# Kernel optimization log

Hardware: AMD Instinct MI355X
Metric: run time of the kernel (lower is better)

Reference implementation:

```python
import jax, jax.numpy as jnp
import numpy as np

B, C, M = 2048, 1, 80  # M = max_object; matrices are (M+1)x(M+1)


def setup_inputs() -> dict:
    key = jax.random.key(0)
    k1, k2, k3, k4 = jax.random.split(key, 4)
    inp = {
        "input": jax.random.normal(k1, (B, C, M + 1, M + 1), dtype=jnp.float32),
        "target": jax.random.randint(k2, (B, C, M + 1, M + 1), 0, 2, dtype=jnp.int32),
        "mask0": jax.random.randint(k3, (B, C, M + 1), 0, 2, dtype=jnp.int32),
        "mask1": jax.random.randint(k4, (B, C, M + 1), 0, 2, dtype=jnp.int32),
        "outputs": 0,
        "current_fair_labels": 0,
        "next_fair_labels": 0,
    }
    return inp


def reference(input, target, mask0, mask1, outputs, current_fair_labels, next_fair_labels):
    f32 = jnp.float32
    m0 = mask0.astype(f32)[:, :, :, None]   # [B,C,M+1,1] (row mask, broadcast over cols)
    m1 = mask1.astype(f32)[:, :, None, :]   # [B,C,1,M+1] (col mask, broadcast over rows)
    mask_region = m0 * m1                    # [B,C,M+1,M+1]
    mask_region_pre = mask_region.at[:, :, M, :].set(0.0)   # zero last row
    mask_region_next = mask_region.at[:, :, :, M].set(0.0)  # zero last col
    mask_region_union = mask_region_pre * mask_region_next

    input_pre = jax.nn.softmax(mask_region_pre * input, axis=3)
    input_next = jax.nn.softmax(mask_region_next * input, axis=2)
    input_all = input_pre.at[:, :, :M, :M].set(
        jnp.maximum(input_pre, input_next)[:, :, :M, :M])

    t = target.astype(jnp.bool_).astype(f32)
    target_pre = mask_region_pre * t
    target_next = mask_region_next * t
    target_union = mask_region_union * t

    target_num = t.sum()
    n_pre = target_pre.sum()
    n_next = target_next.sum()
    n_union = target_union.sum()

    s_pre = -(target_pre * jnp.log(input_pre)).sum()
    loss_pre = jnp.where(n_pre > 0, s_pre / n_pre, s_pre)

    s_next = -(target_next * jnp.log(input_next)).sum()
    loss_next = jnp.where(n_next > 0, s_next / n_next, s_next)

    s_all = -(target_pre * jnp.log(input_all)).sum()
    loss = jnp.where((n_pre > 0) & (n_next > 0), s_all / n_pre, s_all)

    # |1 - p_pre - (1 - p_next)| == |p_next - p_pre|
    s_sim = (target_union * jnp.abs(input_next - input_pre)).sum()
    loss_similarity = jnp.where(n_union > 0, s_sim / target_num, s_sim)

    # accuracy on "pre" direction (argmax over cols, drop last row)
    idx_t_pre = jnp.argmax(target_pre, axis=3)[:, :, :-1]
    indexes_pre = jnp.argmax(input_all, axis=3)[:, :, :-1]
    mpre = mask0.astype(f32)[:, :, :-1]
    n_mpre = mpre.sum()
    s_acc_pre = ((indexes_pre == idx_t_pre).astype(f32) * mpre).sum()
    accuracy_pre = jnp.where(n_mpre > 0, s_acc_pre / n_mpre, s_acc_pre + 1.0)

    # accuracy on "next" direction (argmax over rows, drop last col)
    idx_t_next = jnp.argmax(target_next, axis=2)[:, :, :-1]
    indexes_next = jnp.argmax(input_next, axis=2)[:, :, :-1]
    mnext = mask1.astype(f32)[:, :, :-1]
    n_mnext = mnext.sum()
    s_acc_next = ((indexes_next == idx_t_next).astype(f32) * mnext).sum()
    accuracy_next = jnp.where(n_mnext > 0, s_acc_next / n_mnext, s_acc_next + 1.0)

    total = (loss_pre + loss_next + loss + loss_similarity) / 4.0
    return (loss_pre, loss_next, loss_similarity, total,
            accuracy_pre, accuracy_next, (accuracy_pre + accuracy_next) / 2.0,
            indexes_pre)
```

## Files before the change

kernel.cpp:

```cpp
#include <hip/hip_runtime.h>

#define M1 81
#define MSZ 80
#define NEL (M1 * M1)
#define NTW ((NEL + 31) / 32)
#define NACC 12
#define BIGKC 1.0e30f
#define LOG81 4.394449154672439f
#define INV81 0.012345679012345678f


__global__ __launch_bounds__(512, 8) void sst_main(
    const float* __restrict__ input,
    const int* __restrict__ target,
    const int* __restrict__ mask0,
    const int* __restrict__ mask1,
    float* __restrict__ out_idx,
    float* __restrict__ part,
    int slices)
{
    __shared__ float s_x[NEL];
    __shared__ unsigned s_tb[NTW];
    __shared__ float s_m0[M1], s_m1[M1];
    __shared__ float s_kc[M1];
    __shared__ float s_invc[M1];
    __shared__ float s_pA[486];
    __shared__ float s_pC[480];
    __shared__ float s_pV[486];
    __shared__ unsigned char s_pI[486];
    __shared__ unsigned char s_pT[486];
    __shared__ unsigned s_m1w[4];
    __shared__ float s_wv[8][NACC];

    const int tid   = threadIdx.x;
    const int lane  = tid & 63;
    const int w     = tid >> 6;
    const int slice = blockIdx.x;
    const size_t base = (size_t)slice * NEL;

    if (tid < M1) s_m0[tid] = (float)mask0[slice * M1 + tid];
    else if (tid >= 128 && tid < 128 + M1) s_m1[tid - 128] = (float)mask1[slice * M1 + (tid - 128)];

    float a[NACC];
#pragma unroll
    for (int k = 0; k < NACC; ++k) a[k] = 0.0f;

    for (int i = tid; i < NEL; i += 512) {
        s_x[i] = input[base + i];
        const int tv = target[base + i];
        a[0] += (tv != 0) ? 1.0f : 0.0f;
        unsigned long long m = __ballot(tv != 0);
        if (lane == 0) {
            const int w2 = (i >> 5) & ~1;
            s_tb[w2] = (unsigned)m;
            if (w2 + 1 < NTW) s_tb[w2 + 1] = (unsigned)(m >> 32);
        }
    }
    __syncthreads();

    if (w == 0) {
        const unsigned long long m = __ballot(s_m1[lane] != 0.0f);
        if (lane == 0) { s_m1w[0] = (unsigned)m; s_m1w[1] = (unsigned)(m >> 32); }
    } else if (w == 1) {
        float v = 0.0f;
        if (lane < 17) v = s_m1[64 + lane];
        const unsigned long long m = __ballot(v != 0.0f);
        if (lane == 0) { s_m1w[2] = (unsigned)m; s_m1w[3] = 0u; }
    }

    if (tid < 486) {
        const int c = tid / 6, j = tid - 6 * (tid / 6);
        const int r0 = j * 13 + ((j < 3) ? j : 3);
        const int len = (j < 3) ? 14 : 13;
        const float m1c = s_m1[c];
        const float mcol = (c == MSZ) ? 0.0f : m1c;
        float cs = 0.0f, bv = -1.0f;
        int bi = r0, ct = 127;
        for (int i = 0; i < len; ++i) {
            const int r = r0 + i;
            const int idx = r * M1 + c;
            const float m0r = s_m0[r];
            const float z = m1c * m0r * s_x[idx];
            const float e = __expf(z);
            s_x[idx] = z;
            cs += e;
            if (e > bv) { bv = e; bi = r; }
            const unsigned tb = (s_tb[idx >> 5] >> (idx & 31)) & 1u;
            if (ct == 127 && tb != 0u && (mcol * m0r) != 0.0f) ct = r;
        }
        s_pA[tid] = cs; s_pV[tid] = bv;
        s_pI[tid] = (unsigned char)bi; s_pT[tid] = (unsigned char)ct;
    }
    __syncthreads();

    if (tid < 480) {
        const int r = tid / 6, j = tid - 6 * (tid / 6);
        const int c0 = j * 13 + ((j < 3) ? j : 3);
        const int len = (j < 3) ? 14 : 13;
        const int rb = r * M1 + c0;
        float rs = 0.0f;
        for (int i = 0; i < len; ++i) rs += __expf(s_x[rb + i]);
        s_pC[tid] = rs;
    } else {
        const int u = tid - 480;
        for (int c = u; c < M1; c += 32) {
            if (c < MSZ) {
                const int b = 6 * c;
                float cs = 0.0f;
#pragma unroll
                for (int k = 0; k < 6; ++k) cs += s_pA[b + k];
                float bv = s_pV[b]; int bi = s_pI[b];
#pragma unroll
                for (int k = 1; k < 6; ++k) {
                    const float v = s_pV[b + k];
                    if (v > bv) { bv = v; bi = s_pI[b + k]; }
                }
                int ct = 127;
#pragma unroll
                for (int k = 0; k < 6; ++k) ct = min(ct, (int)s_pT[b + k]);
                if (ct == 127) ct = 0;
                s_kc[c] = __logf(cs);
                s_invc[c] = 1.0f / cs;
                const float m1c = s_m1[c];
                a[9]  += (bi == ct) ? m1c : 0.0f;
                a[11] += m1c;
            } else {
                s_kc[c] = BIGKC; s_invc[c] = INV81;
            }
        }
    }
    __syncthreads();

    if (tid < 480) {
        const int r = tid / 6, j = tid - 6 * (tid / 6);
        const int c0 = j * 13 + ((j < 3) ? j : 3);
        const int len = (j < 3) ? 14 : 13;
        const int rb = r * M1;
        const int pb = 6 * r;
        const float rs = s_pC[pb] + s_pC[pb + 1] + s_pC[pb + 2]
                       + s_pC[pb + 3] + s_pC[pb + 4] + s_pC[pb + 5];
        const float lr = __logf(rs), invr = 1.0f / rs;
        const float m0f = s_m0[r];

        const int bp = rb + c0;
        const unsigned long long tw64 =
            ((unsigned long long)s_tb[(bp >> 5) + 1] << 32) | s_tb[bp >> 5];
        const int mp0 = c0 >> 5;
        const unsigned long long mw64 =
            ((unsigned long long)s_m1w[mp0 + 1] << 32) | s_m1w[mp0];
        const unsigned lenmask = (1u << len) - 1u;
        unsigned wb = (unsigned)(tw64 >> (bp & 31)) & (unsigned)(mw64 >> (c0 & 31)) & lenmask;
        if (m0f == 0.0f) wb = 0u;

        const unsigned w3 = (j == 5) ? (wb & 0x0FFFu) : wb;
        a[1] += (float)__popc(wb);
        a[2] += (float)__popc(w3);
        a[3] += (float)__popc(w3);
        const int ti = wb ? (c0 + __ffs(wb) - 1) : 127;

        float bv = -3.402823466e38f; int bi = c0;
        for (int i = 0; i < len; ++i) {
            const int c = c0 + i;
            const float val = s_x[rb + c] - fminf(lr, s_kc[c]);
            if (val > bv) { bv = val; bi = c; }
        }
        unsigned wl = wb;
        while (wl) {
            const int b = __ffs(wl) - 1; wl &= wl - 1u;
            const int c = c0 + b;
            const float z = s_x[rb + c];
            const float kc = s_kc[c];
            a[4] += lr - z;
            a[6] += fminf(lr, kc) - z;
            const bool c80 = (c == MSZ);
            a[5] += c80 ? 0.0f : (kc - z);
            const float e = c80 ? 0.0f : __expf(z);
            a[7] = fmaf(e, fabsf(s_invc[c] - invr), a[7]);
        }
        s_pV[tid] = bv; s_pI[tid] = (unsigned char)bi; s_pT[tid] = (unsigned char)ti;
    } else if (tid < 486) {
        const int j = tid - 480;
        const int c0 = j * 13 + ((j < 3) ? j : 3);
        const int len = (j < 3) ? 14 : 13;
        const int rb = MSZ * M1;
        const float m80 = s_m0[MSZ];
        const int bp = rb + c0;
        const unsigned long long tw64 =
            ((unsigned long long)s_tb[(bp >> 5) + 1] << 32) | s_tb[bp >> 5];
        const int mp0 = c0 >> 5;
        const unsigned long long mw64 =
            ((unsigned long long)s_m1w[mp0 + 1] << 32) | s_m1w[mp0];
        const unsigned lenmask = (1u << len) - 1u;
        unsigned wb = (unsigned)(tw64 >> (bp & 31)) & (unsigned)(mw64 >> (c0 & 31)) & lenmask;
        if (m80 == 0.0f) wb = 0u;
        if (j == 5) wb &= 0x0FFFu;
        a[2] += (float)__popc(wb);
        while (wb) {
            const int b = __ffs(wb) - 1; wb &= wb - 1u;
            const int c = c0 + b;
            a[5] += s_kc[c] - s_x[rb + c];
        }
    }
    __syncthreads();

    if (tid < MSZ) {
        const int b = 6 * tid;
        float bv = s_pV[b]; int bi = s_pI[b];
#pragma unroll
        for (int k = 1; k < 6; ++k) {
            const float v = s_pV[b + k];
            if (v > bv) { bv = v; bi = s_pI[b + k]; }
        }
        int ti = 127;
#pragma unroll
        for (int k = 0; k < 6; ++k) ti = min(ti, (int)s_pT[b + k]);
        if (ti == 127) ti = 0;
        out_idx[(size_t)slice * MSZ + tid] = (float)bi;
        const float m0f = s_m0[tid];
        a[8]  += (bi == ti) ? m0f : 0.0f;
        a[10] += m0f;
    }

#pragma unroll
    for (int k = 0; k < NACC; ++k) {
        float v = a[k];
        for (int off = 32; off > 0; off >>= 1) v += __shfl_down(v, off);
        if (lane == 0) s_wv[w][k] = v;
    }
    __syncthreads();
    if (tid < NACC) {
        float s = 0.0f;
#pragma unroll
        for (int ww = 0; ww < 8; ++ww) s += s_wv[ww][tid];
        part[(size_t)tid * slices + slice] = s;
    }
}

__global__ __launch_bounds__(256) void sst_final(
    const float* __restrict__ part, int slices, float* __restrict__ out)
{
    __shared__ double s_part[4][NACC];
    const int tid = threadIdx.x;
    double l[NACC];
#pragma unroll
    for (int k = 0; k < NACC; ++k) l[k] = 0.0;
    for (int s = tid; s < slices; s += 256) {
#pragma unroll
        for (int k = 0; k < NACC; ++k) l[k] += (double)part[(size_t)k * slices + s];
    }
#pragma unroll
    for (int k = 0; k < NACC; ++k) {
        double v = l[k];
        for (int off = 32; off > 0; off >>= 1) v += __shfl_down(v, off);
        if ((tid & 63) == 0) s_part[tid >> 6][k] = v;
    }
    __syncthreads();
    if (tid == 0) {
        double g[NACC];
#pragma unroll
        for (int k = 0; k < NACC; ++k)
            g[k] = s_part[0][k] + s_part[1][k] + s_part[2][k] + s_part[3][k];
        const double tnum = g[0], npre = g[1], nnext = g[2], nunion = g[3];
        const double spre = g[4], snext = g[5], sall = g[6], ssim = g[7];
        const double accp = g[8], accn = g[9], nmp = g[10], nmn = g[11];
        const double loss_pre  = (npre > 0.0) ? spre / npre : spre;
        const double loss_next = (nnext > 0.0) ? snext / nnext : snext;
        const double loss      = (npre > 0.0 && nnext > 0.0) ? sall / npre : sall;
        const double loss_sim  = (nunion > 0.0) ? ssim / tnum : ssim;
        const double total = (loss_pre + loss_next + loss + loss_sim) * 0.25;
        const double ap = (nmp > 0.0) ? accp / nmp : accp + 1.0;
        const double an = (nmn > 0.0) ? accn / nmn : accn + 1.0;
        out[0] = (float)loss_pre;
        out[1] = (float)loss_next;
        out[2] = (float)loss_sim;
        out[3] = (float)total;
        out[4] = (float)ap;
        out[5] = (float)an;
        out[6] = (float)((ap + an) * 0.5);
    }
}

extern "C" void kernel_launch(void* const* d_in, const int* in_sizes, int n_in,
                              void* d_out, int out_size, void* d_ws, size_t ws_size,
                              hipStream_t stream) {
    const float* input  = (const float*)d_in[0];
    const int*   target = (const int*)d_in[1];
    const int*   mask0  = (const int*)d_in[2];
    const int*   mask1  = (const int*)d_in[3];
    float* out = (float*)d_out;
    float* part = (float*)d_ws;

    const int slices = in_sizes[0] / NEL;

    sst_main<<<slices, 512, 0, stream>>>(input, target, mask0, mask1, out + 7, part, slices);
    sst_final<<<1, 256, 0, stream>>>(part, slices, out);
}
```

Baseline: 167.4 us.

## Vectorize input loads, store exp in shared memory, defer target bitmask build

The input tile is now loaded with aligned float4 reads, using a per-slice shared-memory offset so the vector loads line up. Target values are prefetched into registers and turned into the ballot bitmask after the column pass, so those loads overlap with compute. Shared memory now holds exp(z) instead of z, which removes the repeated exp in the row-sum pass at the cost of a log in the sparse target loop. The first target row of each column for the column accuracy now comes from shared-memory atomicMin during the row pass rather than a per-element bit test in the column pass. The atomics and the extra register pressure from 13 prefetched ints could hurt occupancy.

```diff
diff --git a/kernel.cpp b/kernel.cpp
--- a/kernel.cpp
+++ b/kernel.cpp
@@ -6,8 +6,6 @@
 #define NTW ((NEL + 31) / 32)
 #define NACC 12
 #define BIGKC 1.0e30f
-#define LOG81 4.394449154672439f
-#define INV81 0.012345679012345678f
 
 
 __global__ __launch_bounds__(512, 8) void sst_main(
@@ -19,7 +17,7 @@
     float* __restrict__ part,
     int slices)
 {
-    __shared__ float s_x[NEL];
+    __shared__ __align__(16) float s_xraw[NEL + 4];
     __shared__ unsigned s_tb[NTW];
     __shared__ float s_m0[M1], s_m1[M1];
     __shared__ float s_kc[M1];
@@ -29,6 +27,8 @@
     __shared__ float s_pV[486];
     __shared__ unsigned char s_pI[486];
     __shared__ unsigned char s_pT[486];
+    __shared__ unsigned char s_ci[MSZ];
+    __shared__ int s_ct[MSZ];
     __shared__ unsigned s_m1w[4];
     __shared__ float s_wv[8][NACC];
 
@@ -38,23 +38,29 @@
     const int slice = blockIdx.x;
     const size_t base = (size_t)slice * NEL;
 
+    float* sx = s_xraw + (slice & 3);
+    const int h = (4 - (slice & 3)) & 3;
+
     if (tid < M1) s_m0[tid] = (float)mask0[slice * M1 + tid];
     else if (tid >= 128 && tid < 128 + M1) s_m1[tid - 128] = (float)mask1[slice * M1 + (tid - 128)];
+    if (tid >= 256 && tid < 256 + MSZ) s_ct[tid - 256] = 0x7fffffff;
 
     float a[NACC];
 #pragma unroll
     for (int k = 0; k < NACC; ++k) a[k] = 0.0f;
 
-    for (int i = tid; i < NEL; i += 512) {
-        s_x[i] = input[base + i];
-        const int tv = target[base + i];
-        a[0] += (tv != 0) ? 1.0f : 0.0f;
-        unsigned long long m = __ballot(tv != 0);
-        if (lane == 0) {
-            const int w2 = (i >> 5) & ~1;
-            s_tb[w2] = (unsigned)m;
-            if (w2 + 1 < NTW) s_tb[w2 + 1] = (unsigned)(m >> 32);
-        }
+    const int n4 = (NEL - h) >> 2;
+    const float4* in4 = (const float4*)(input + base + h);
+    for (int i = tid; i < n4; i += 512)
+        *(float4*)(sx + h + (i << 2)) = in4[i];
+    if (tid < h) sx[tid] = input[base + tid];
+    for (int i = h + (n4 << 2) + tid; i < NEL; i += 512) sx[i] = input[base + i];
+
+    int tpre[13];
+#pragma unroll
+    for (int k = 0; k < 13; ++k) {
+        const int i = tid + (k << 9);
+        tpre[k] = (i < NEL) ? target[base + i] : 0;
     }
     __syncthreads();
 
@@ -73,23 +79,32 @@
         const int r0 = j * 13 + ((j < 3) ? j : 3);
         const int len = (j < 3) ? 14 : 13;
         const float m1c = s_m1[c];
-        const float mcol = (c == MSZ) ? 0.0f : m1c;
         float cs = 0.0f, bv = -1.0f;
-        int bi = r0, ct = 127;
-        for (int i = 0; i < len; ++i) {
+        int bi = r0;
+        int idx = r0 * M1 + c;
+        for (int i = 0; i < len; ++i, idx += M1) {
             const int r = r0 + i;
-            const int idx = r * M1 + c;
-            const float m0r = s_m0[r];
-            const float z = m1c * m0r * s_x[idx];
+            const float z = m1c * s_m0[r] * sx[idx];
             const float e = __expf(z);
-            s_x[idx] = z;
+            sx[idx] = e;
             cs += e;
             if (e > bv) { bv = e; bi = r; }
-            const unsigned tb = (s_tb[idx >> 5] >> (idx & 31)) & 1u;
-            if (ct == 127 && tb != 0u && (mcol * m0r) != 0.0f) ct = r;
-        }
-        s_pA[tid] = cs; s_pV[tid] = bv;
-        s_pI[tid] = (unsigned char)bi; s_pT[tid] = (unsigned char)ct;
+        }
+        s_pA[tid] = cs; s_pV[tid] = bv; s_pI[tid] = (unsigned char)bi;
+    }
+
+#pragma unroll
+    for (int k = 0; k < 13; ++k) {
+        const int i = tid + (k << 9);
+        if (i < NEL) {
+            const unsigned long long m = __ballot(tpre[k] != 0);
+            if (lane == 0) {
+                a[0] += (float)__popcll(m);
+                const int w2 = (i >> 5) & ~1;
+                s_tb[w2] = (unsigned)m;
+                if (w2 + 1 < NTW) s_tb[w2 + 1] = (unsigned)(m >> 32);
+            }
+        }
     }
     __syncthreads();
 
@@ -99,7 +114,7 @@
         const int len = (j < 3) ? 14 : 13;
         const int rb = r * M1 + c0;
         float rs = 0.0f;
-        for (int i = 0; i < len; ++i) rs += __expf(s_x[rb + i]);
+        for (int i = 0; i < len; ++i) rs += sx[rb + i];
         s_pC[tid] = rs;
     } else {
         const int u = tid - 480;
@@ -115,17 +130,12 @@
                     const float v = s_pV[b + k];
                     if (v > bv) { bv = v; bi = s_pI[b + k]; }
                 }
-                int ct = 127;
-#pragma unroll
-                for (int k = 0; k < 6; ++k) ct = min(ct, (int)s_pT[b + k]);
-                if (ct == 127) ct = 0;
                 s_kc[c] = __logf(cs);
                 s_invc[c] = 1.0f / cs;
-                const float m1c = s_m1[c];
-                a[9]  += (bi == ct) ? m1c : 0.0f;
-                a[11] += m1c;
+                s_ci[c] = (unsigned char)bi;
             } else {
-                s_kc[c] = BIGKC; s_invc[c] = INV81;
+                s_kc[c] = BIGKC;
+                s_invc[c] = 0.0f;
             }
         }
     }
@@ -158,24 +168,25 @@
         a[3] += (float)__popc(w3);
         const int ti = wb ? (c0 + __ffs(wb) - 1) : 127;
 
-        float bv = -3.402823466e38f; int bi = c0;
+        float bv = -1.0f; int bi = c0;
         for (int i = 0; i < len; ++i) {
             const int c = c0 + i;
-            const float val = s_x[rb + c] - fminf(lr, s_kc[c]);
+            const float val = sx[rb + c] * fmaxf(invr, s_invc[c]);
             if (val > bv) { bv = val; bi = c; }
         }
         unsigned wl = wb;
         while (wl) {
             const int b = __ffs(wl) - 1; wl &= wl - 1u;
             const int c = c0 + b;
-            const float z = s_x[rb + c];
-            const float kc = s_kc[c];
+            const float e = sx[rb + c];
+            const float z = __logf(e);
             a[4] += lr - z;
-            a[6] += fminf(lr, kc) - z;
-            const bool c80 = (c == MSZ);
-            a[5] += c80 ? 0.0f : (kc - z);
-            const float e = c80 ? 0.0f : __expf(z);
-            a[7] = fmaf(e, fabsf(s_invc[c] - invr), a[7]);
+            a[6] += fminf(lr, s_kc[c]) - z;
+            if (c != MSZ) {
+                a[5] += s_kc[c] - z;
+                a[7] = fmaf(e, fabsf(s_invc[c] - invr), a[7]);
+                atomicMin(&s_ct[c], r);
+            }
         }
         s_pV[tid] = bv; s_pI[tid] = (unsigned char)bi; s_pT[tid] = (unsigned char)ti;
     } else if (tid < 486) {
@@ -198,7 +209,8 @@
         while (wb) {
             const int b = __ffs(wb) - 1; wb &= wb - 1u;
             const int c = c0 + b;
-            a[5] += s_kc[c] - s_x[rb + c];
+            a[5] += s_kc[c] - __logf(sx[rb + c]);
+            atomicMin(&s_ct[c], MSZ);
         }
     }
     __syncthreads();
@@ -219,6 +231,14 @@
         const float m0f = s_m0[tid];
         a[8]  += (bi == ti) ? m0f : 0.0f;
         a[10] += m0f;
+    } else if (tid >= 128 && tid < 128 + MSZ) {
+        const int c = tid - 128;
+        const int ctv = s_ct[c];
+        const int ti = (ctv == 0x7fffffff) ? 0 : ctv;
+        const int bi = (int)s_ci[c];
+        const float m1c = s_m1[c];
+        a[9]  += (bi == ti) ? m1c : 0.0f;
+        a[11] += m1c;
     }
 
 #pragma unroll
```

After: 165.3 us. No clear change (-1.3%).
